# Performance work log

Measured on AMD Instinct MI355X. Metric: run time of the kernel, lower is better.

Reference implementation:

```python
import jax, jax.numpy as jnp
import numpy as np

IN_FEATURE = 256
OUT_FEATURE = 128
ALPHA = 0.5  # LeakyReLU negative slope
NEG_BIG = -9e15


def setup_inputs() -> dict:
    key = jax.random.key(0)
    k1, k2, k3, k4 = jax.random.split(key, 4)
    N = 8192
    x = jax.random.normal(k1, (N, IN_FEATURE), dtype=jnp.float32)
    adj = jax.random.randint(k2, (N, N), 0, 2, dtype=jnp.int32)
    stdv = 1.0 / np.sqrt(OUT_FEATURE)
    W = jax.random.uniform(k3, (IN_FEATURE, OUT_FEATURE), dtype=jnp.float32,
                           minval=-stdv, maxval=stdv)
    a = jax.random.uniform(k4, (2 * OUT_FEATURE, 1), dtype=jnp.float32,
                           minval=-stdv, maxval=stdv)
    return {"input": x, "adj": adj, "W": W, "a": a}


def reference(input, adj, W, a):
    # h: [N, F_out]
    h = input @ W
    # Additive attention: cat([h_i, h_j]) @ a == h_i @ a1 + h_j @ a2
    a1 = a[:OUT_FEATURE, 0]   # [F_out]
    a2 = a[OUT_FEATURE:, 0]   # [F_out]
    f1 = h @ a1               # [N]  (row / source contribution)
    f2 = h @ a2               # [N]  (col / target contribution)
    e = jax.nn.leaky_relu(f1[:, None] + f2[None, :], negative_slope=ALPHA)  # [N, N]
    scores = jnp.where(adj > 0, e, NEG_BIG)
    attention = jax.nn.softmax(scores, axis=1)  # [N, N]
    h_prime = attention @ h                     # [N, F_out]
    return jax.nn.elu(h_prime)
```

## Files before the change

kernel.cpp:

```cpp
#include <hip/hip_runtime.h>

#define N_NODES 8192
#define IN_F 256
#define OUT_F 128
#define ALPHA 0.5f
#define JC 4
#define JCHUNK 2048
#define STEPS 64

using short8 = __attribute__((ext_vector_type(8))) short;
using f32x4  = __attribute__((ext_vector_type(4))) float;

__device__ __forceinline__ unsigned short f2bf(float f){
  unsigned int u = __float_as_uint(f);
  u += 0x7fffu + ((u >> 16) & 1u);
  return (unsigned short)(u >> 16);
}

__global__ __launch_bounds__(256) void k_h(const float* __restrict__ x,
                                           const float* __restrict__ W,
                                           float* __restrict__ h){
  __shared__ float xs[16*IN_F];
  const int tid = threadIdx.x;
  const int r0 = blockIdx.x * 16;
  const float4* xg = (const float4*)(x + (size_t)r0*IN_F);
  float4* xl = (float4*)xs;
  #pragma unroll
  for(int i=0;i<4;i++) xl[tid + i*256] = xg[tid + i*256];
  __syncthreads();
  const int wave = tid >> 6, lane = tid & 63;
  float2 acc[4];
  #pragma unroll
  for(int j=0;j<4;j++){ acc[j].x = 0.f; acc[j].y = 0.f; }
  const float2* Wp = (const float2*)W;
  for(int k4=0;k4<IN_F;k4+=4){
    float4 xq[4];
    #pragma unroll
    for(int j=0;j<4;j++) xq[j] = *(const float4*)&xs[(wave*4+j)*IN_F + k4];
    #pragma unroll
    for(int kk=0;kk<4;kk++){
      float2 wv = Wp[(size_t)(k4+kk)*64 + lane];
      #pragma unroll
      for(int j=0;j<4;j++){
        float xv = kk==0?xq[j].x : kk==1?xq[j].y : kk==2?xq[j].z : xq[j].w;
        acc[j].x += xv*wv.x; acc[j].y += xv*wv.y;
      }
    }
  }
  #pragma unroll
  for(int j=0;j<4;j++)
    *(float2*)(h + (size_t)(r0 + wave*4 + j)*OUT_F + lane*2) = acc[j];
}

__global__ __launch_bounds__(256) void k_f(const float* __restrict__ h,
                                           const float* __restrict__ a,
                                           float* __restrict__ f1,
                                           float* __restrict__ f2){
  const int wave = threadIdx.x >> 6, lane = threadIdx.x & 63;
  const int row = blockIdx.x*4 + wave;
  float2 hv = ((const float2*)(h + (size_t)row*OUT_F))[lane];
  float2 a1 = ((const float2*)a)[lane];
  float2 a2 = ((const float2*)(a + OUT_F))[lane];
  float s1 = hv.x*a1.x + hv.y*a1.y;
  float s2 = hv.x*a2.x + hv.y*a2.y;
  #pragma unroll
  for(int off=32; off; off>>=1){
    s1 += __shfl_down(s1, off);
    s2 += __shfl_down(s2, off);
  }
  if(lane == 0){ f1[row] = s1; f2[row] = s2; }
}

#define LDW 132
__global__ __launch_bounds__(256) void k_pack(const float* __restrict__ h,
                                              unsigned short* __restrict__ P){
  __shared__ float ld[32*LDW];
  const int tid = threadIdx.x;
  const int kb = blockIdx.x, j0 = kb*32;
  #pragma unroll
  for(int i=0;i<4;i++){
    int idx = tid + i*256;
    int row = idx >> 5, c4 = (idx & 31)*4;
    *(float4*)&ld[row*LDW + c4] = *(const float4*)(h + (size_t)(j0+row)*OUT_F + c4);
  }
  __syncthreads();
  #pragma unroll
  for(int i=0;i<2;i++){
    int o = tid*2 + i;
    int c = o >> 6, lane = o & 63;
    int q = lane >> 4, n = lane & 15;
    short8 v;
    #pragma unroll
    for(int t=0;t<8;t++) v[t] = (short)f2bf(ld[(q*8+t)*LDW + c*16 + n]);
    *(short8*)(P + ((size_t)(kb*8 + c)*64 + lane)*8) = v;
  }
}

__global__ __launch_bounds__(256, 2) void k_attn(const int* __restrict__ adj,
    const unsigned short* __restrict__ P,
    const float* __restrict__ f1, const float* __restrict__ f2,
    float* __restrict__ part, float* __restrict__ denp){
  const int tid = threadIdx.x;
  const int wave = tid >> 6, lane = tid & 63;
  const int m = lane & 15, q = lane >> 4;
  const int jc = blockIdx.x;
  const int r0 = blockIdx.y*64 + wave*16;
  const int jbase = jc * JCHUNK;
  const int kb0 = jbase >> 5;
  const float rowf1 = f1[r0 + m];
  const int* ap = adj + (size_t)(r0 + m)*N_NODES + jbase + q*8;
  const float* f2p = f2 + jbase + q*8;
  const short8* Pv = (const short8*)P;

  f32x4 acc[8];
  #pragma unroll
  for(int c=0;c<8;c++) acc[c] = (f32x4){0,0,0,0};
  float den = 0.f;

  int4 a0 = *(const int4*)(ap);
  int4 a1 = *(const int4*)(ap + 4);

  #pragma unroll 2
  for(int s=0; s<STEPS; s++){
    int4 b0, b1;
    if(s+1 < STEPS){
      b0 = *(const int4*)(ap + (s+1)*32);
      b1 = *(const int4*)(ap + (s+1)*32 + 4);
    }
    float4 fa = *(const float4*)(f2p + s*32);
    float4 fb = *(const float4*)(f2p + s*32 + 4);
    short8 af;
    {
      float tv, ev, w;
      #define WELEM(slot, aval, f2v)                       \
        tv = rowf1 + (f2v);                                \
        ev = tv > 0.f ? tv : ALPHA*tv;                     \
        w  = __expf(ev);                                   \
        w  = ((aval) > 0) ? w : 0.f;                       \
        den += w;                                          \
        af[slot] = (short)f2bf(w);
      WELEM(0, a0.x, fa.x) WELEM(1, a0.y, fa.y)
      WELEM(2, a0.z, fa.z) WELEM(3, a0.w, fa.w)
      WELEM(4, a1.x, fb.x) WELEM(5, a1.y, fb.y)
      WELEM(6, a1.z, fb.z) WELEM(7, a1.w, fb.w)
      #undef WELEM
    }
    const short8* Bb = Pv + ((size_t)(kb0 + s)*512 + lane);
    #pragma unroll
    for(int c=0;c<8;c++)
      acc[c] = __builtin_amdgcn_mfma_f32_16x16x32_bf16(af, Bb[c*64], acc[c], 0,0,0);
    a0 = b0; a1 = b1;
  }

  den += __shfl_down(den, 32);
  den += __shfl_down(den, 16);
  if(lane < 16) denp[(size_t)jc*N_NODES + r0 + lane] = den;

  float* pp = part + (size_t)jc*N_NODES*OUT_F;
  #pragma unroll
  for(int c=0;c<8;c++){
    #pragma unroll
    for(int reg=0;reg<4;reg++)
      pp[(size_t)(r0 + q*4 + reg)*OUT_F + c*16 + m] = acc[c][reg];
  }
}

__global__ __launch_bounds__(256) void k_out(const float* __restrict__ part,
    const float* __restrict__ denp, float* __restrict__ out){
  const int idx = blockIdx.x*256 + threadIdx.x;
  const int r = idx >> 7;
  float v = 0.f, d = 0.f;
  #pragma unroll
  for(int p=0;p<JC;p++){
    v += part[(size_t)p*N_NODES*OUT_F + idx];
    d += denp[(size_t)p*N_NODES + r];
  }
  v /= d;
  out[idx] = v > 0.f ? v : (__expf(v) - 1.f);
}

extern "C" void kernel_launch(void* const* d_in, const int* in_sizes, int n_in,
                              void* d_out, int out_size, void* d_ws, size_t ws_size,
                              hipStream_t stream){
  const float* x   = (const float*)d_in[0];
  const int*   adj = (const int*)d_in[1];
  const float* W   = (const float*)d_in[2];
  const float* a   = (const float*)d_in[3];
  char* ws = (char*)d_ws;
  float* h            = (float*)ws;
  unsigned short* P   = (unsigned short*)(ws + (4u<<20));
  float* f1           = (float*)(ws + (6u<<20));
  float* f2           = (float*)(ws + (6u<<20) + (32u<<10));
  float* part         = (float*)(ws + (8u<<20));
  float* denp         = (float*)(ws + (24u<<20));
  float* out          = (float*)d_out;

  k_h<<<512, 256, 0, stream>>>(x, W, h);
  k_f<<<2048, 256, 0, stream>>>(h, a, f1, f2);
  k_pack<<<256, 256, 0, stream>>>(h, P);
  k_attn<<<dim3(JC,128), 256, 0, stream>>>(adj, P, f1, f2, part, denp);
  k_out<<<(N_NODES*OUT_F)/256, 256, 0, stream>>>(part, denp, out);
}
```

Before: 494.5 us.

## Stage packed h tiles in LDS and process two row tiles per wave

Each wave now computes 32 rows instead of 16, reusing every B fragment for two MFMAs. The packed h tiles are staged in shared memory per round so all four waves share them instead of each loading from global. The column split doubles to 8 chunks to keep the block count the same, and the denominator buffer moves to fit the larger partial sums. This adds register pressure, 64 KB of LDS per block and more partial-sum traffic for the final reduction.

```diff
diff --git a/kernel.cpp b/kernel.cpp
--- a/kernel.cpp
+++ b/kernel.cpp
@@ -4,9 +4,10 @@
 #define IN_F 256
 #define OUT_F 128
 #define ALPHA 0.5f
-#define JC 4
-#define JCHUNK 2048
-#define STEPS 64
+#define JC 8
+#define KCHUNK 1024
+#define ROUNDS 4
+#define RSTEPS 8
 
 using short8 = __attribute__((ext_vector_type(8))) short;
 using f32x4  = __attribute__((ext_vector_type(4))) float;
@@ -100,68 +101,95 @@
     const unsigned short* __restrict__ P,
     const float* __restrict__ f1, const float* __restrict__ f2,
     float* __restrict__ part, float* __restrict__ denp){
+  __shared__ __align__(16) short Blds[32768];
   const int tid = threadIdx.x;
   const int wave = tid >> 6, lane = tid & 63;
   const int m = lane & 15, q = lane >> 4;
   const int jc = blockIdx.x;
-  const int r0 = blockIdx.y*64 + wave*16;
-  const int jbase = jc * JCHUNK;
-  const int kb0 = jbase >> 5;
-  const float rowf1 = f1[r0 + m];
-  const int* ap = adj + (size_t)(r0 + m)*N_NODES + jbase + q*8;
-  const float* f2p = f2 + jbase + q*8;
+  const int rb = blockIdx.y;
+  const int r0w = rb*128 + wave*32;
+  const int kb0 = jc * (KCHUNK/32);
+  const float rf1a = f1[r0w + m];
+  const float rf1b = f1[r0w + 16 + m];
+  const int* ap0 = adj + (size_t)(r0w + m)*N_NODES + jc*KCHUNK + q*8;
+  const int* ap1 = ap0 + (size_t)16*N_NODES;
+  const float* f2p = f2 + jc*KCHUNK + q*8;
   const short8* Pv = (const short8*)P;
 
-  f32x4 acc[8];
-  #pragma unroll
-  for(int c=0;c<8;c++) acc[c] = (f32x4){0,0,0,0};
-  float den = 0.f;
-
-  int4 a0 = *(const int4*)(ap);
-  int4 a1 = *(const int4*)(ap + 4);
-
-  #pragma unroll 2
-  for(int s=0; s<STEPS; s++){
-    int4 b0, b1;
-    if(s+1 < STEPS){
-      b0 = *(const int4*)(ap + (s+1)*32);
-      b1 = *(const int4*)(ap + (s+1)*32 + 4);
-    }
-    float4 fa = *(const float4*)(f2p + s*32);
-    float4 fb = *(const float4*)(f2p + s*32 + 4);
-    short8 af;
-    {
-      float tv, ev, w;
-      #define WELEM(slot, aval, f2v)                       \
-        tv = rowf1 + (f2v);                                \
-        ev = tv > 0.f ? tv : ALPHA*tv;                     \
-        w  = __expf(ev);                                   \
-        w  = ((aval) > 0) ? w : 0.f;                       \
-        den += w;                                          \
-        af[slot] = (short)f2bf(w);
-      WELEM(0, a0.x, fa.x) WELEM(1, a0.y, fa.y)
-      WELEM(2, a0.z, fa.z) WELEM(3, a0.w, fa.w)
-      WELEM(4, a1.x, fb.x) WELEM(5, a1.y, fb.y)
-      WELEM(6, a1.z, fb.z) WELEM(7, a1.w, fb.w)
-      #undef WELEM
-    }
-    const short8* Bb = Pv + ((size_t)(kb0 + s)*512 + lane);
-    #pragma unroll
-    for(int c=0;c<8;c++)
-      acc[c] = __builtin_amdgcn_mfma_f32_16x16x32_bf16(af, Bb[c*64], acc[c], 0,0,0);
-    a0 = b0; a1 = b1;
-  }
-
-  den += __shfl_down(den, 32);
-  den += __shfl_down(den, 16);
-  if(lane < 16) denp[(size_t)jc*N_NODES + r0 + lane] = den;
-
+  f32x4 acc0[8], acc1[8];
+  #pragma unroll
+  for(int c=0;c<8;c++){ acc0[c] = (f32x4){0,0,0,0}; acc1[c] = (f32x4){0,0,0,0}; }
+  float den0 = 0.f, den1 = 0.f;
+
+  int4 A00 = *(const int4*)(ap0);
+  int4 A01 = *(const int4*)(ap0 + 4);
+  int4 A10 = *(const int4*)(ap1);
+  int4 A11 = *(const int4*)(ap1 + 4);
+
+  auto welem8 = [&](const int4& a, const int4& b, const float4& fa,
+                    const float4& fb, float rf1, float& den) -> short8 {
+    short8 af; float tv, ev, w;
+    #define WE(slot, av, fv)                               \
+      tv = rf1 + (fv);                                     \
+      ev = tv > 0.f ? tv : ALPHA*tv;                       \
+      w  = __expf(ev);                                     \
+      w  = ((av) > 0) ? w : 0.f;                           \
+      den += w;                                            \
+      af[slot] = (short)f2bf(w);
+    WE(0,a.x,fa.x) WE(1,a.y,fa.y) WE(2,a.z,fa.z) WE(3,a.w,fa.w)
+    WE(4,b.x,fb.x) WE(5,b.y,fb.y) WE(6,b.z,fb.z) WE(7,b.w,fb.w)
+    #undef WE
+    return af;
+  };
+
+  for(int rd=0; rd<ROUNDS; rd++){
+    const short8* Ps = Pv + (size_t)(kb0 + rd*8) * 512;
+    short8* Bl8 = (short8*)Blds;
+    #pragma unroll
+    for(int i=0;i<16;i++){
+      int idx = i*256 + tid;
+      Bl8[idx] = Ps[idx];
+    }
+    __syncthreads();
+    for(int s=0; s<RSTEPS; s++){
+      const int gs = rd*RSTEPS + s;
+      int4 B00=A00, B01=A01, B10=A10, B11=A11;
+      if(gs+1 < ROUNDS*RSTEPS){
+        B00 = *(const int4*)(ap0 + (gs+1)*32);
+        B01 = *(const int4*)(ap0 + (gs+1)*32 + 4);
+        B10 = *(const int4*)(ap1 + (gs+1)*32);
+        B11 = *(const int4*)(ap1 + (gs+1)*32 + 4);
+      }
+      float4 fa = *(const float4*)(f2p + gs*32);
+      float4 fb = *(const float4*)(f2p + gs*32 + 4);
+      short8 af0 = welem8(A00, A01, fa, fb, rf1a, den0);
+      short8 af1 = welem8(A10, A11, fa, fb, rf1b, den1);
+      const short8* Bl = (const short8*)Blds + (s*512 + lane);
+      #pragma unroll
+      for(int c=0;c<8;c++){
+        short8 Bf = Bl[c*64];
+        acc0[c] = __builtin_amdgcn_mfma_f32_16x16x32_bf16(af0, Bf, acc0[c], 0,0,0);
+        acc1[c] = __builtin_amdgcn_mfma_f32_16x16x32_bf16(af1, Bf, acc1[c], 0,0,0);
+      }
+      A00=B00; A01=B01; A10=B10; A11=B11;
+    }
+    __syncthreads();
+  }
+
+  den0 += __shfl_down(den0, 32); den0 += __shfl_down(den0, 16);
+  den1 += __shfl_down(den1, 32); den1 += __shfl_down(den1, 16);
+  if(lane < 16){
+    denp[(size_t)jc*N_NODES + r0w + lane]      = den0;
+    denp[(size_t)jc*N_NODES + r0w + 16 + lane] = den1;
+  }
   float* pp = part + (size_t)jc*N_NODES*OUT_F;
   #pragma unroll
   for(int c=0;c<8;c++){
     #pragma unroll
-    for(int reg=0;reg<4;reg++)
-      pp[(size_t)(r0 + q*4 + reg)*OUT_F + c*16 + m] = acc[c][reg];
+    for(int reg=0;reg<4;reg++){
+      pp[(size_t)(r0w + q*4 + reg)*OUT_F      + c*16 + m] = acc0[c][reg];
+      pp[(size_t)(r0w + 16 + q*4 + reg)*OUT_F + c*16 + m] = acc1[c][reg];
+    }
   }
 }
 
@@ -192,12 +220,12 @@
   float* f1           = (float*)(ws + (6u<<20));
   float* f2           = (float*)(ws + (6u<<20) + (32u<<10));
   float* part         = (float*)(ws + (8u<<20));
-  float* denp         = (float*)(ws + (24u<<20));
+  float* denp         = (float*)(ws + (40u<<20));
   float* out          = (float*)d_out;
 
   k_h<<<512, 256, 0, stream>>>(x, W, h);
   k_f<<<2048, 256, 0, stream>>>(h, a, f1, f2);
   k_pack<<<256, 256, 0, stream>>>(h, P);
-  k_attn<<<dim3(JC,128), 256, 0, stream>>>(adj, P, f1, f2, part, denp);
+  k_attn<<<dim3(JC,64), 256, 0, stream>>>(adj, P, f1, f2, part, denp);
   k_out<<<(N_NODES*OUT_F)/256, 256, 0, stream>>>(part, denp, out);
 }
```

New measurement: 458.3 us. 1.08x faster.
